# Kernel tuning notes

Hardware: AMD Instinct MI355X
Metric: run time of the kernel (lower is better)

The kernel has to match this reference:

```python
import jax, jax.numpy as jnp
import numpy as np

B, S, D = 2, 2048, 2048
H = 16
HD = D // (2 * H)          # 64, per-map head dim
LBDA_INIT = 0.8


def apply_rope_real(x, cos, sin):
    # x: [B, H, S, HD]; cos/sin: [S, HD//2]
    b, h, s, d = x.shape
    xr = x.reshape(b, h, s, d // 2, 2)
    x1, x2 = xr[..., 0], xr[..., 1]
    c = cos[None, None, :, :]
    sn = sin[None, None, :, :]
    o1 = x1 * c - x2 * sn
    o2 = x1 * sn + x2 * c
    return jnp.stack([o1, o2], axis=-1).reshape(b, h, s, d)


def setup_inputs() -> dict:
    key = jax.random.key(0)
    ks = jax.random.split(key, 6)
    x = jax.random.normal(ks[0], (B, S, D), dtype=jnp.float32)
    # causal additive mask [1,1,S,S]
    causal = jnp.tril(jnp.ones((S, S), dtype=bool))
    mask = jnp.where(causal, 0.0, -1e9).astype(jnp.float32)[None, None]
    # RoPE tables for half_head_dim = HD//2
    inv_freq = 1.0 / (10000.0 ** (jnp.arange(0, HD // 2, dtype=jnp.float32) / (HD // 2)))
    t = jnp.arange(S, dtype=jnp.float32)
    freqs = t[:, None] * inv_freq[None, :]          # [S, HD//2]
    cos, sin = jnp.cos(freqs), jnp.sin(freqs)
    W_qkv = jax.random.normal(ks[1], (D, HD * H * 2 * 3), dtype=jnp.float32) * (D ** -0.5)
    W_o = jax.random.normal(ks[2], (D, D), dtype=jnp.float32) * (D ** -0.5)
    ln_gamma = jnp.ones((H, 2 * HD), dtype=jnp.float32)
    ln_beta = jnp.zeros((H, 2 * HD), dtype=jnp.float32)
    lbda = jnp.float32(0.5)
    return {"x": x, "mask": mask, "cos": cos, "sin": sin, "W_qkv": W_qkv,
            "W_o": W_o, "ln_gamma": ln_gamma, "ln_beta": ln_beta, "lbda": lbda}


def reference(x, mask, cos, sin, W_qkv, W_o, ln_gamma, ln_beta, lbda):
    b, s, d = x.shape
    scale = HD ** -0.5
    qkv = x @ W_qkv                                  # [B, S, 6*H*HD]
    q, k, v = jnp.split(qkv, 3, axis=-1)
    # [B, S, H, 2*HD] -> [B, H, S, 2*HD]
    q = q.reshape(b, s, H, 2 * HD).transpose(0, 2, 1, 3)
    k = k.reshape(b, s, H, 2 * HD).transpose(0, 2, 1, 3)
    v = v.reshape(b, s, H, 2 * HD).transpose(0, 2, 1, 3)
    q1, q2 = jnp.split(q, 2, axis=-1)
    k1, k2 = jnp.split(k, 2, axis=-1)
    q1, k1 = apply_rope_real(q1, cos, sin), apply_rope_real(k1, cos, sin)
    q2, k2 = apply_rope_real(q2, cos, sin), apply_rope_real(k2, cos, sin)
    qk1 = jnp.einsum('bhqd,bhkd->bhqk', q1, k1) * scale + mask
    qk2 = jnp.einsum('bhqd,bhkd->bhqk', q2, k2) * scale + mask
    a = jax.nn.softmax(qk1, axis=-1) - lbda * jax.nn.softmax(qk2, axis=-1)
    out = jnp.einsum('bhqk,bhkd->bhqd', a, v)        # [B, H, S, 2*HD]
    # per-head LayerNorm over last dim
    mu = out.mean(-1, keepdims=True)
    var = out.var(-1, keepdims=True)
    out = (out - mu) * jax.lax.rsqrt(var + 1e-5)
    out = out * ln_gamma[None, :, None, :] + ln_beta[None, :, None, :]
    out = out * (1.0 - LBDA_INIT)
    out = out.transpose(0, 2, 1, 3).reshape(b, s, d)
    return out @ W_o
```

## Files before the change

kernel.cpp:

```cpp
#include <hip/hip_runtime.h>
#include <hip/hip_bf16.h>
#include <cstdint>
#include <cstddef>

#define S_LEN 2048
#define NHEAD 16
#define BATCH 2

typedef unsigned short u16;
typedef __attribute__((ext_vector_type(8))) unsigned short u16x8;
typedef __attribute__((ext_vector_type(8))) short s16x8;
typedef __attribute__((ext_vector_type(4))) float f32x4;

__device__ __forceinline__ u16 bfb(float x) {
    __hip_bfloat16 b = __float2bfloat16(x);
    u16 u; __builtin_memcpy(&u, &b, 2); return u;
}
__device__ __forceinline__ float bff(u16 u) {
    __hip_bfloat16 b; __builtin_memcpy(&b, &u, 2); return __bfloat162float(b);
}

#define BMFMA(A, B, C) __builtin_amdgcn_mfma_f32_16x16x32_bf16( \
    __builtin_bit_cast(s16x8, A), __builtin_bit_cast(s16x8, B), C, 0, 0, 0)

template<int MODE>
__global__ __launch_bounds__(256)
void gemm_bf16s(const float* __restrict__ A, const float* __restrict__ B,
                float* __restrict__ C, float* __restrict__ qo,
                u16* __restrict__ khh, u16* __restrict__ khl,
                u16* __restrict__ vhh, u16* __restrict__ vhl,
                const float* __restrict__ ct, const float* __restrict__ st,
                int M, int N, int K)
{
    __shared__ u16 Ah[128 * 40];
    __shared__ u16 Al[128 * 40];
    __shared__ u16 Bh[128 * 40];
    __shared__ u16 Bl[128 * 40];

    const int tid  = threadIdx.x;
    const int lane = tid & 63;
    const int wid  = tid >> 6;
    const int wrow = wid >> 1, wcol = wid & 1;
    const int m0 = blockIdx.y * 128, n0 = blockIdx.x * 128;
    const int l15 = lane & 15;
    const int lg  = lane >> 4;
    const int bkb = tid & 7;
    const int bng = tid >> 3;

    f32x4 acc[4][4];
    #pragma unroll
    for (int mt = 0; mt < 4; mt++)
        #pragma unroll
        for (int nt = 0; nt < 4; nt++)
            acc[mt][nt] = (f32x4){0.f, 0.f, 0.f, 0.f};

    for (int k0 = 0; k0 < K; k0 += 32) {
        float4 av[4], bv[4];
        int am[4], ak[4];
        #pragma unroll
        for (int f = 0; f < 4; f++) {
            const int ai = f * 256 + tid;
            am[f] = ai >> 3;
            ak[f] = (ai & 7) * 4;
            av[f] = *(const float4*)(A + (size_t)(m0 + am[f]) * K + k0 + ak[f]);
            bv[f] = *(const float4*)(B + (size_t)(k0 + bkb * 4 + f) * N + n0 + bng * 4);
        }
        __syncthreads();
        #pragma unroll
        for (int f = 0; f < 4; f++) {
            const float* ap = reinterpret_cast<const float*>(&av[f]);
            const int off = am[f] * 40 + ak[f];
            #pragma unroll
            for (int e = 0; e < 4; e++) {
                const u16 hu = bfb(ap[e]);
                Ah[off + e] = hu;
                Al[off + e] = bfb(ap[e] - bff(hu));
            }
        }
        #pragma unroll
        for (int e = 0; e < 4; e++) {
            const int off = (bng * 4 + e) * 40 + bkb * 4;
            #pragma unroll
            for (int f = 0; f < 4; f++) {
                const float x = reinterpret_cast<const float*>(&bv[f])[e];
                const u16 hu = bfb(x);
                Bh[off + f] = hu;
                Bl[off + f] = bfb(x - bff(hu));
            }
        }
        __syncthreads();

        u16x8 bh[4], bl[4];
        #pragma unroll
        for (int nt = 0; nt < 4; nt++) {
            const int off = (wcol * 64 + nt * 16 + l15) * 40 + lg * 8;
            bh[nt] = *(const u16x8*)&Bh[off];
            bl[nt] = *(const u16x8*)&Bl[off];
        }
        #pragma unroll
        for (int mt = 0; mt < 4; mt++) {
            const int off = (wrow * 64 + mt * 16 + l15) * 40 + lg * 8;
            const u16x8 ah = *(const u16x8*)&Ah[off];
            const u16x8 al = *(const u16x8*)&Al[off];
            #pragma unroll
            for (int nt = 0; nt < 4; nt++) {
                acc[mt][nt] = BMFMA(al, bh[nt], acc[mt][nt]);
                acc[mt][nt] = BMFMA(ah, bl[nt], acc[mt][nt]);
                acc[mt][nt] = BMFMA(ah, bh[nt], acc[mt][nt]);
            }
        }
    }

    #pragma unroll
    for (int mt = 0; mt < 4; mt++) {
        #pragma unroll
        for (int r = 0; r < 4; r++) {
            const int row = m0 + wrow * 64 + mt * 16 + lg * 4 + r;
            if (MODE == 0) {
                #pragma unroll
                for (int nt = 0; nt < 4; nt++) {
                    const int col = n0 + wcol * 64 + nt * 16 + l15;
                    C[(size_t)row * N + col] = acc[mt][nt][r];
                }
            } else {
                const int b = row >> 11, s = row & 2047;
                #pragma unroll
                for (int nt = 0; nt < 4; nt++) {
                    const int col = n0 + wcol * 64 + nt * 16 + l15;
                    const int which = col >> 11;
                    const int cc = col & 2047;
                    const int hh = cc >> 7, d = cc & 127;
                    float v = acc[mt][nt][r];
                    const float pv = __shfl_xor(v, 1);
                    if (which < 2) {
                        const int p = (d & 63) >> 1;
                        const float c  = ct[s * 32 + p];
                        const float sn = st[s * 32 + p];
                        v = (d & 1) ? (pv * sn + v * c) : (v * c - pv * sn);
                    }
                    const size_t idx =
                        ((size_t)(b * NHEAD + hh) * S_LEN + s) * 128 + d;
                    if (which == 0) {
                        qo[idx] = v;
                    } else if (which == 1) {
                        const u16 hu = bfb(v);
                        khh[idx] = hu;
                        khl[idx] = bfb(v - bff(hu));
                    } else {
                        const u16 hu = bfb(v);
                        vhh[idx] = hu;
                        vhl[idx] = bfb(v - bff(hu));
                    }
                }
            }
        }
    }
}

__global__ __launch_bounds__(256)
void transpose_v(const u16* __restrict__ vhh, const u16* __restrict__ vhl,
                 u16* __restrict__ vth, u16* __restrict__ vtl)
{
    __shared__ unsigned int T[64][130];
    const int tid = threadIdx.x;
    const int s0 = blockIdx.x * 64;
    const int bh = blockIdx.y;
    const size_t base = (size_t)bh * S_LEN * 128;

    #pragma unroll
    for (int i = 0; i < 4; i++) {
        const int f = i * 256 + tid;
        const int r = f >> 4, c8 = (f & 15) * 8;
        const u16x8 h = *(const u16x8*)(vhh + base + (size_t)(s0 + r) * 128 + c8);
        const u16x8 l = *(const u16x8*)(vhl + base + (size_t)(s0 + r) * 128 + c8);
        #pragma unroll
        for (int e = 0; e < 8; e++)
            T[r][c8 + e] = ((unsigned int)h[e] << 16) | l[e];
    }
    __syncthreads();

    const int d = tid >> 1, sc = (tid & 1) * 32;
    u16x8 oh[4], ol[4];
    #pragma unroll
    for (int j = 0; j < 32; j++) {
        const unsigned int w = T[sc + j][d];
        oh[j >> 3][j & 7] = (u16)(w >> 16);
        ol[j >> 3][j & 7] = (u16)(w & 0xffff);
    }
    const size_t ob = ((size_t)bh * 128 + d) * S_LEN + s0 + sc;
    #pragma unroll
    for (int k = 0; k < 4; k++) {
        *(u16x8*)(vth + ob + k * 8) = oh[k];
        *(u16x8*)(vtl + ob + k * 8) = ol[k];
    }
}

__global__ __launch_bounds__(256, 2)
void diff_attn_mfma(const float* __restrict__ qh,
                    const u16* __restrict__ khh, const u16* __restrict__ khl,
                    const u16* __restrict__ vth, const u16* __restrict__ vtl,
                    const float* __restrict__ gamma, const float* __restrict__ beta,
                    const float* __restrict__ lbda_p, float* __restrict__ att)
{
    __shared__ u16 sKh[64 * 128];
    __shared__ u16 sKl[64 * 128];
    __shared__ u16 sVh[128 * 64];
    __shared__ u16 sVl[128 * 64];
    __shared__ u16 sP[4][16 * 64];

    const int tid = threadIdx.x, lane = tid & 63, wid = tid >> 6;
    const int l15 = lane & 15, lg = lane >> 4;
    const int qt = blockIdx.x, h = blockIdx.y, b = blockIdx.z;
    const int bh = b * NHEAD + h;
    const int q0w = qt * 64 + wid * 16;

    u16x8 qfh[2][2], qfl[2][2];
    {
        const float* Qrow = qh + ((size_t)bh * S_LEN + q0w + l15) * 128;
        #pragma unroll
        for (int h12 = 0; h12 < 2; h12++)
            #pragma unroll
            for (int ks = 0; ks < 2; ks++) {
                const int d0 = h12 * 64 + ks * 32 + lg * 8;
                const float4 x = *(const float4*)(Qrow + d0);
                const float4 y = *(const float4*)(Qrow + d0 + 4);
                const float xs[8] = {x.x, x.y, x.z, x.w, y.x, y.y, y.z, y.w};
                u16x8 hh, ll;
                #pragma unroll
                for (int e = 0; e < 8; e++) {
                    const float v = xs[e] * 0.125f;
                    const u16 hu = bfb(v);
                    hh[e] = hu;
                    ll[e] = bfb(v - bff(hu));
                }
                qfh[h12][ks] = hh;
                qfl[h12][ks] = ll;
            }
    }

    f32x4 o1[8], o2[8];
    #pragma unroll
    for (int i = 0; i < 8; i++) {
        o1[i] = (f32x4){0.f, 0.f, 0.f, 0.f};
        o2[i] = (f32x4){0.f, 0.f, 0.f, 0.f};
    }
    float l1[4] = {0.f, 0.f, 0.f, 0.f}, l2[4] = {0.f, 0.f, 0.f, 0.f};

    for (int kt = 0; kt <= qt; kt++) {
        const int kv0 = kt * 64;
        u16x8 rkh[4], rkl[4], rvh[4], rvl[4];
        #pragma unroll
        for (int i = 0; i < 4; i++) {
            const int f = i * 256 + tid;
            {
                const int kv = f >> 4, blk = f & 15;
                const size_t g = ((size_t)bh * S_LEN + kv0 + kv) * 128 + blk * 8;
                rkh[i] = *(const u16x8*)(khh + g);
                rkl[i] = *(const u16x8*)(khl + g);
            }
            {
                const int dd = f >> 3, vb = f & 7;
                const size_t g = ((size_t)bh * 128 + dd) * S_LEN + kv0 + vb * 8;
                rvh[i] = *(const u16x8*)(vth + g);
                rvl[i] = *(const u16x8*)(vtl + g);
            }
        }
        __syncthreads();
        #pragma unroll
        for (int i = 0; i < 4; i++) {
            const int f = i * 256 + tid;
            {
                const int kv = f >> 4, blk = f & 15;
                const int a = kv * 128 + ((blk ^ (kv & 7)) * 8);
                *(u16x8*)&sKh[a] = rkh[i];
                *(u16x8*)&sKl[a] = rkl[i];
            }
            {
                const int dd = f >> 3, vb = f & 7;
                const int a = dd * 64 + ((vb ^ (dd & 7)) * 8);
                *(u16x8*)&sVh[a] = rvh[i];
                *(u16x8*)&sVl[a] = rvl[i];
            }
        }
        __syncthreads();

        f32x4 s1[4], s2[4];
        #pragma unroll
        for (int nt = 0; nt < 4; nt++) {
            s1[nt] = (f32x4){0.f, 0.f, 0.f, 0.f};
            s2[nt] = (f32x4){0.f, 0.f, 0.f, 0.f};
        }
        #pragma unroll
        for (int ks = 0; ks < 2; ks++)
            #pragma unroll
            for (int nt = 0; nt < 4; nt++) {
                const int kvr = nt * 16 + l15;
                const int cb = l15 & 7;
                {
                    const int a = kvr * 128 + (((ks * 4 + lg) ^ cb) * 8);
                    const u16x8 kbh = *(const u16x8*)&sKh[a];
                    const u16x8 kbl = *(const u16x8*)&sKl[a];
                    s1[nt] = BMFMA(qfl[0][ks], kbh, s1[nt]);
                    s1[nt] = BMFMA(qfh[0][ks], kbl, s1[nt]);
                    s1[nt] = BMFMA(qfh[0][ks], kbh, s1[nt]);
                }
                {
                    const int a = kvr * 128 + (((8 + ks * 4 + lg) ^ cb) * 8);
                    const u16x8 kbh = *(const u16x8*)&sKh[a];
                    const u16x8 kbl = *(const u16x8*)&sKl[a];
                    s2[nt] = BMFMA(qfl[1][ks], kbh, s2[nt]);
                    s2[nt] = BMFMA(qfh[1][ks], kbl, s2[nt]);
                    s2[nt] = BMFMA(qfh[1][ks], kbh, s2[nt]);
                }
            }

        const bool diag = (kt == qt);
        float p1[4][4], p2[4][4];
        #pragma unroll
        for (int nt = 0; nt < 4; nt++)
            #pragma unroll
            for (int r = 0; r < 4; r++) {
                float e1 = __expf(s1[nt][r]);
                float e2 = __expf(s2[nt][r]);
                if (diag) {
                    const int kv = kv0 + nt * 16 + l15;
                    const int qq = q0w + lg * 4 + r;
                    if (kv > qq) { e1 = 0.f; e2 = 0.f; }
                }
                p1[nt][r] = e1;
                p2[nt][r] = e2;
            }
        #pragma unroll
        for (int r = 0; r < 4; r++) {
            float a1 = p1[0][r] + p1[1][r] + p1[2][r] + p1[3][r];
            float a2 = p2[0][r] + p2[1][r] + p2[2][r] + p2[3][r];
            #pragma unroll
            for (int off = 1; off < 16; off <<= 1) {
                a1 += __shfl_xor(a1, off);
                a2 += __shfl_xor(a2, off);
            }
            l1[r] += a1;
            l2[r] += a2;
        }

        u16* myP = &sP[wid][0];
        #pragma unroll
        for (int nt = 0; nt < 4; nt++)
            #pragma unroll
            for (int r = 0; r < 4; r++) {
                const int q = lg * 4 + r, kv = l15 + nt * 16;
                myP[q * 64 + (((kv >> 3) ^ (q & 7)) * 8) + (kv & 7)] =
                    bfb(p1[nt][r]);
            }
        {
            u16x8 pf0 = *(const u16x8*)&myP[l15 * 64 + ((lg ^ (l15 & 7)) * 8)];
            u16x8 pf1 = *(const u16x8*)&myP[l15 * 64 + (((4 + lg) ^ (l15 & 7)) * 8)];
            #pragma unroll
            for (int nt = 0; nt < 8; nt++) {
                const int dr = nt * 16 + l15;
                const int cb = l15 & 7;
                {
                    const int a = dr * 64 + ((lg ^ cb) * 8);
                    o1[nt] = BMFMA(pf0, *(const u16x8*)&sVh[a], o1[nt]);
                    o1[nt] = BMFMA(pf0, *(const u16x8*)&sVl[a], o1[nt]);
                }
                {
                    const int a = dr * 64 + (((4 + lg) ^ cb) * 8);
                    o1[nt] = BMFMA(pf1, *(const u16x8*)&sVh[a], o1[nt]);
                    o1[nt] = BMFMA(pf1, *(const u16x8*)&sVl[a], o1[nt]);
                }
            }
        }
        #pragma unroll
        for (int nt = 0; nt < 4; nt++)
            #pragma unroll
            for (int r = 0; r < 4; r++) {
                const int q = lg * 4 + r, kv = l15 + nt * 16;
                myP[q * 64 + (((kv >> 3) ^ (q & 7)) * 8) + (kv & 7)] =
                    bfb(p2[nt][r]);
            }
        {
            u16x8 pf0 = *(const u16x8*)&myP[l15 * 64 + ((lg ^ (l15 & 7)) * 8)];
            u16x8 pf1 = *(const u16x8*)&myP[l15 * 64 + (((4 + lg) ^ (l15 & 7)) * 8)];
            #pragma unroll
            for (int nt = 0; nt < 8; nt++) {
                const int dr = nt * 16 + l15;
                const int cb = l15 & 7;
                {
                    const int a = dr * 64 + ((lg ^ cb) * 8);
                    o2[nt] = BMFMA(pf0, *(const u16x8*)&sVh[a], o2[nt]);
                    o2[nt] = BMFMA(pf0, *(const u16x8*)&sVl[a], o2[nt]);
                }
                {
                    const int a = dr * 64 + (((4 + lg) ^ cb) * 8);
                    o2[nt] = BMFMA(pf1, *(const u16x8*)&sVh[a], o2[nt]);
                    o2[nt] = BMFMA(pf1, *(const u16x8*)&sVl[a], o2[nt]);
                }
            }
        }
    }

    const float lam = lbda_p[0];
    float inv1[4], inv2[4];
    #pragma unroll
    for (int r = 0; r < 4; r++) {
        inv1[r] = 1.f / l1[r];
        inv2[r] = lam / l2[r];
    }
    float o[8][4];
    float sum[4] = {0.f, 0.f, 0.f, 0.f}, ssq[4] = {0.f, 0.f, 0.f, 0.f};
    #pragma unroll
    for (int nt = 0; nt < 8; nt++)
        #pragma unroll
        for (int r = 0; r < 4; r++) {
            const float v = o1[nt][r] * inv1[r] - o2[nt][r] * inv2[r];
            o[nt][r] = v;
            sum[r] += v;
            ssq[r] += v * v;
        }
    #pragma unroll
    for (int r = 0; r < 4; r++)
        #pragma unroll
        for (int off = 1; off < 16; off <<= 1) {
            sum[r] += __shfl_xor(sum[r], off);
            ssq[r] += __shfl_xor(ssq[r], off);
        }
    #pragma unroll
    for (int nt = 0; nt < 8; nt++) {
        const int d = nt * 16 + l15;
        const float gm = gamma[h * 128 + d];
        const float bt = beta[h * 128 + d];
        #pragma unroll
        for (int r = 0; r < 4; r++) {
            const float mu = sum[r] * (1.f / 128.f);
            const float var = ssq[r] * (1.f / 128.f) - mu * mu;
            const float rs = rsqrtf(var + 1e-5f);
            const int s = q0w + lg * 4 + r;
            att[((size_t)(b * S_LEN + s)) * 2048 + h * 128 + d] =
                ((o[nt][r] - mu) * rs * gm + bt) * 0.2f;
        }
    }
}

extern "C" void kernel_launch(void* const* d_in, const int* in_sizes, int n_in,
                              void* d_out, int out_size, void* d_ws, size_t ws_size,
                              hipStream_t stream)
{
    const float* x     = (const float*)d_in[0];
    const float* cosT  = (const float*)d_in[2];
    const float* sinT  = (const float*)d_in[3];
    const float* W_qkv = (const float*)d_in[4];
    const float* W_o   = (const float*)d_in[5];
    const float* gamma = (const float*)d_in[6];
    const float* beta  = (const float*)d_in[7];
    const float* lbda  = (const float*)d_in[8];
    float* out = (float*)d_out;

    float* ws = (float*)d_ws;
    const size_t HS = (size_t)BATCH * NHEAD * S_LEN * 128;
    float* qh  = ws;
    u16* khh   = (u16*)(ws + HS);
    u16* khl   = khh + HS;
    u16* vhh   = (u16*)(ws + 2 * HS);
    u16* vhl   = vhh + HS;
    u16* vth   = (u16*)(ws + 3 * HS);
    u16* vtl   = vth + HS;
    float* att = ws + 2 * HS;

    {
        dim3 grid(6144 / 128, 4096 / 128);
        gemm_bf16s<1><<<grid, 256, 0, stream>>>(x, W_qkv, nullptr, qh,
                                                khh, khl, vhh, vhl,
                                                cosT, sinT, 4096, 6144, 2048);
    }
    {
        dim3 grid(S_LEN / 64, BATCH * NHEAD);
        transpose_v<<<grid, 256, 0, stream>>>(vhh, vhl, vth, vtl);
    }
    {
        dim3 grid(S_LEN / 64, NHEAD, BATCH);
        diff_attn_mfma<<<grid, 256, 0, stream>>>(qh, khh, khl, vth, vtl,
                                                 gamma, beta, lbda, att);
    }
    {
        dim3 grid(2048 / 128, 4096 / 128);
        gemm_bf16s<0><<<grid, 256, 0, stream>>>(att, W_o, out, nullptr,
                                                nullptr, nullptr, nullptr, nullptr,
                                                nullptr, nullptr, 4096, 2048, 2048);
    }
}
```

Before: 981.7 us.

## Pre-split GEMM operands into bf16 hi/lo buffers instead of per-tile conversion

Adds conversion kernels that split x and a transposed W_o into bf16 high/low pairs once, and makes the attention kernel emit its output directly as bf16 hi/lo. The QKV and output GEMMs then load pre-split bf16 operands with vectorized LDS stores, removing repeated float-to-bf16 splitting inside every tile iteration. This costs extra passes over x and W_o and reuses workspace regions whose earlier contents are already dead.

```diff
diff --git a/kernel.cpp b/kernel.cpp
--- a/kernel.cpp
+++ b/kernel.cpp
@@ -9,6 +9,7 @@
 
 typedef unsigned short u16;
 typedef __attribute__((ext_vector_type(8))) unsigned short u16x8;
+typedef __attribute__((ext_vector_type(4))) unsigned short u16x4;
 typedef __attribute__((ext_vector_type(8))) short s16x8;
 typedef __attribute__((ext_vector_type(4))) float f32x4;
 
@@ -23,15 +24,64 @@
 #define BMFMA(A, B, C) __builtin_amdgcn_mfma_f32_16x16x32_bf16( \
     __builtin_bit_cast(s16x8, A), __builtin_bit_cast(s16x8, B), C, 0, 0, 0)
 
-template<int MODE>
 __global__ __launch_bounds__(256)
-void gemm_bf16s(const float* __restrict__ A, const float* __restrict__ B,
-                float* __restrict__ C, float* __restrict__ qo,
-                u16* __restrict__ khh, u16* __restrict__ khl,
-                u16* __restrict__ vhh, u16* __restrict__ vhl,
-                const float* __restrict__ ct, const float* __restrict__ st,
-                int M, int N, int K)
+void convert_split(const float* __restrict__ in, u16* __restrict__ oh,
+                   u16* __restrict__ ol)
 {
+    const size_t base = ((size_t)blockIdx.x * 256 + threadIdx.x) * 8;
+    const float4 a = *(const float4*)(in + base);
+    const float4 b = *(const float4*)(in + base + 4);
+    const float xs[8] = {a.x, a.y, a.z, a.w, b.x, b.y, b.z, b.w};
+    u16x8 hh, ll;
+    #pragma unroll
+    for (int e = 0; e < 8; e++) {
+        const u16 hu = bfb(xs[e]);
+        hh[e] = hu;
+        ll[e] = bfb(xs[e] - bff(hu));
+    }
+    *(u16x8*)(oh + base) = hh;
+    *(u16x8*)(ol + base) = ll;
+}
+
+__global__ __launch_bounds__(256)
+void convert_wot(const float* __restrict__ W, u16* __restrict__ bh,
+                 u16* __restrict__ bl)
+{
+    __shared__ float T[64][65];
+    const int tid = threadIdx.x;
+    const int n0 = blockIdx.x * 64, k0 = blockIdx.y * 64;
+    #pragma unroll
+    for (int i = 0; i < 4; i++) {
+        const int c = i * 256 + tid;
+        const int r = c >> 4, n4 = (c & 15) * 4;
+        *(float4*)&T[r][n4] = *(const float4*)(W + (size_t)(k0 + r) * 2048 + n0 + n4);
+    }
+    __syncthreads();
+    #pragma unroll
+    for (int i = 0; i < 4; i++) {
+        const int c = i * 256 + tid;
+        const int n = c >> 4, k4 = (c & 15) * 4;
+        u16 h[4], l[4];
+        #pragma unroll
+        for (int j = 0; j < 4; j++) {
+            const float v = T[k4 + j][n];
+            h[j] = bfb(v);
+            l[j] = bfb(v - bff(h[j]));
+        }
+        const size_t off = (size_t)(n0 + n) * 2048 + k0 + k4;
+        *(u16x4*)(bh + off) = (u16x4){h[0], h[1], h[2], h[3]};
+        *(u16x4*)(bl + off) = (u16x4){l[0], l[1], l[2], l[3]};
+    }
+}
+
+__global__ __launch_bounds__(256)
+void gemm_qkv(const u16* __restrict__ xh, const u16* __restrict__ xl,
+              const float* __restrict__ B, float* __restrict__ qo,
+              u16* __restrict__ khh, u16* __restrict__ khl,
+              u16* __restrict__ vhh, u16* __restrict__ vhl,
+              const float* __restrict__ ct, const float* __restrict__ st)
+{
+    const int K = 2048, N = 6144;
     __shared__ u16 Ah[128 * 40];
     __shared__ u16 Al[128 * 40];
     __shared__ u16 Bh[128 * 40];
@@ -55,38 +105,41 @@
             acc[mt][nt] = (f32x4){0.f, 0.f, 0.f, 0.f};
 
     for (int k0 = 0; k0 < K; k0 += 32) {
-        float4 av[4], bv[4];
-        int am[4], ak[4];
-        #pragma unroll
-        for (int f = 0; f < 4; f++) {
-            const int ai = f * 256 + tid;
-            am[f] = ai >> 3;
-            ak[f] = (ai & 7) * 4;
-            av[f] = *(const float4*)(A + (size_t)(m0 + am[f]) * K + k0 + ak[f]);
+        u16x8 rah[2], ral[2];
+        int arow[2], ak8[2];
+        #pragma unroll
+        for (int i = 0; i < 2; i++) {
+            const int c = i * 256 + tid;
+            arow[i] = c >> 2;
+            ak8[i] = (c & 3) * 8;
+            const size_t g = (size_t)(m0 + arow[i]) * K + k0 + ak8[i];
+            rah[i] = *(const u16x8*)(xh + g);
+            ral[i] = *(const u16x8*)(xl + g);
+        }
+        float4 bv[4];
+        #pragma unroll
+        for (int f = 0; f < 4; f++)
             bv[f] = *(const float4*)(B + (size_t)(k0 + bkb * 4 + f) * N + n0 + bng * 4);
-        }
+
         __syncthreads();
         #pragma unroll
-        for (int f = 0; f < 4; f++) {
-            const float* ap = reinterpret_cast<const float*>(&av[f]);
-            const int off = am[f] * 40 + ak[f];
-            #pragma unroll
-            for (int e = 0; e < 4; e++) {
-                const u16 hu = bfb(ap[e]);
-                Ah[off + e] = hu;
-                Al[off + e] = bfb(ap[e] - bff(hu));
-            }
+        for (int i = 0; i < 2; i++) {
+            const int off = arow[i] * 40 + ak8[i];
+            *(u16x8*)&Ah[off] = rah[i];
+            *(u16x8*)&Al[off] = ral[i];
         }
         #pragma unroll
         for (int e = 0; e < 4; e++) {
-            const int off = (bng * 4 + e) * 40 + bkb * 4;
+            u16 h[4], l[4];
             #pragma unroll
             for (int f = 0; f < 4; f++) {
                 const float x = reinterpret_cast<const float*>(&bv[f])[e];
-                const u16 hu = bfb(x);
-                Bh[off + f] = hu;
-                Bl[off + f] = bfb(x - bff(hu));
-            }
+                h[f] = bfb(x);
+                l[f] = bfb(x - bff(h[f]));
+            }
+            const int off = (bng * 4 + e) * 40 + bkb * 4;
+            *(u16x4*)&Bh[off] = (u16x4){h[0], h[1], h[2], h[3]};
+            *(u16x4*)&Bl[off] = (u16x4){l[0], l[1], l[2], l[3]};
         }
         __syncthreads();
 
@@ -116,45 +169,122 @@
         #pragma unroll
         for (int r = 0; r < 4; r++) {
             const int row = m0 + wrow * 64 + mt * 16 + lg * 4 + r;
-            if (MODE == 0) {
-                #pragma unroll
-                for (int nt = 0; nt < 4; nt++) {
-                    const int col = n0 + wcol * 64 + nt * 16 + l15;
-                    C[(size_t)row * N + col] = acc[mt][nt][r];
-                }
-            } else {
-                const int b = row >> 11, s = row & 2047;
-                #pragma unroll
-                for (int nt = 0; nt < 4; nt++) {
-                    const int col = n0 + wcol * 64 + nt * 16 + l15;
-                    const int which = col >> 11;
-                    const int cc = col & 2047;
-                    const int hh = cc >> 7, d = cc & 127;
-                    float v = acc[mt][nt][r];
-                    const float pv = __shfl_xor(v, 1);
-                    if (which < 2) {
-                        const int p = (d & 63) >> 1;
-                        const float c  = ct[s * 32 + p];
-                        const float sn = st[s * 32 + p];
-                        v = (d & 1) ? (pv * sn + v * c) : (v * c - pv * sn);
-                    }
-                    const size_t idx =
-                        ((size_t)(b * NHEAD + hh) * S_LEN + s) * 128 + d;
-                    if (which == 0) {
-                        qo[idx] = v;
-                    } else if (which == 1) {
-                        const u16 hu = bfb(v);
-                        khh[idx] = hu;
-                        khl[idx] = bfb(v - bff(hu));
-                    } else {
-                        const u16 hu = bfb(v);
-                        vhh[idx] = hu;
-                        vhl[idx] = bfb(v - bff(hu));
-                    }
-                }
-            }
-        }
-    }
+            const int b = row >> 11, s = row & 2047;
+            #pragma unroll
+            for (int nt = 0; nt < 4; nt++) {
+                const int col = n0 + wcol * 64 + nt * 16 + l15;
+                const int which = col >> 11;
+                const int cc = col & 2047;
+                const int hh = cc >> 7, d = cc & 127;
+                float v = acc[mt][nt][r];
+                const float pv = __shfl_xor(v, 1);
+                if (which < 2) {
+                    const int p = (d & 63) >> 1;
+                    const float c  = ct[s * 32 + p];
+                    const float sn = st[s * 32 + p];
+                    v = (d & 1) ? (pv * sn + v * c) : (v * c - pv * sn);
+                }
+                const size_t idx = ((size_t)(b * NHEAD + hh) * S_LEN + s) * 128 + d;
+                if (which == 0) {
+                    qo[idx] = v;
+                } else if (which == 1) {
+                    const u16 hu = bfb(v);
+                    khh[idx] = hu;
+                    khl[idx] = bfb(v - bff(hu));
+                } else {
+                    const u16 hu = bfb(v);
+                    vhh[idx] = hu;
+                    vhl[idx] = bfb(v - bff(hu));
+                }
+            }
+        }
+    }
+}
+
+__global__ __launch_bounds__(256)
+void gemm_out(const u16* __restrict__ ah_, const u16* __restrict__ al_,
+              const u16* __restrict__ bth, const u16* __restrict__ btl,
+              float* __restrict__ C)
+{
+    const int K = 2048, N = 2048;
+    __shared__ u16 Ah[128 * 40];
+    __shared__ u16 Al[128 * 40];
+    __shared__ u16 Bh[128 * 40];
+    __shared__ u16 Bl[128 * 40];
+
+    const int tid  = threadIdx.x;
+    const int lane = tid & 63;
+    const int wid  = tid >> 6;
+    const int wrow = wid >> 1, wcol = wid & 1;
+    const int m0 = blockIdx.y * 128, n0 = blockIdx.x * 128;
+    const int l15 = lane & 15;
+    const int lg  = lane >> 4;
+
+    f32x4 acc[4][4];
+    #pragma unroll
+    for (int mt = 0; mt < 4; mt++)
+        #pragma unroll
+        for (int nt = 0; nt < 4; nt++)
+            acc[mt][nt] = (f32x4){0.f, 0.f, 0.f, 0.f};
+
+    for (int k0 = 0; k0 < K; k0 += 32) {
+        u16x8 rah[2], ral[2], rbh[2], rbl[2];
+        int row[2], k8[2];
+        #pragma unroll
+        for (int i = 0; i < 2; i++) {
+            const int c = i * 256 + tid;
+            row[i] = c >> 2;
+            k8[i] = (c & 3) * 8;
+            const size_t ga = (size_t)(m0 + row[i]) * K + k0 + k8[i];
+            const size_t gb = (size_t)(n0 + row[i]) * K + k0 + k8[i];
+            rah[i] = *(const u16x8*)(ah_ + ga);
+            ral[i] = *(const u16x8*)(al_ + ga);
+            rbh[i] = *(const u16x8*)(bth + gb);
+            rbl[i] = *(const u16x8*)(btl + gb);
+        }
+        __syncthreads();
+        #pragma unroll
+        for (int i = 0; i < 2; i++) {
+            const int off = row[i] * 40 + k8[i];
+            *(u16x8*)&Ah[off] = rah[i];
+            *(u16x8*)&Al[off] = ral[i];
+            *(u16x8*)&Bh[off] = rbh[i];
+            *(u16x8*)&Bl[off] = rbl[i];
+        }
+        __syncthreads();
+
+        u16x8 bh[4], bl[4];
+        #pragma unroll
+        for (int nt = 0; nt < 4; nt++) {
+            const int off = (wcol * 64 + nt * 16 + l15) * 40 + lg * 8;
+            bh[nt] = *(const u16x8*)&Bh[off];
+            bl[nt] = *(const u16x8*)&Bl[off];
+        }
+        #pragma unroll
+        for (int mt = 0; mt < 4; mt++) {
+            const int off = (wrow * 64 + mt * 16 + l15) * 40 + lg * 8;
+            const u16x8 ah = *(const u16x8*)&Ah[off];
+            const u16x8 al = *(const u16x8*)&Al[off];
+            #pragma unroll
+            for (int nt = 0; nt < 4; nt++) {
+                acc[mt][nt] = BMFMA(al, bh[nt], acc[mt][nt]);
+                acc[mt][nt] = BMFMA(ah, bl[nt], acc[mt][nt]);
+                acc[mt][nt] = BMFMA(ah, bh[nt], acc[mt][nt]);
+            }
+        }
+    }
+
+    #pragma unroll
+    for (int mt = 0; mt < 4; mt++)
+        #pragma unroll
+        for (int r = 0; r < 4; r++) {
+            const int row = m0 + wrow * 64 + mt * 16 + lg * 4 + r;
+            #pragma unroll
+            for (int nt = 0; nt < 4; nt++) {
+                const int col = n0 + wcol * 64 + nt * 16 + l15;
+                C[(size_t)row * N + col] = acc[mt][nt][r];
+            }
+        }
 }
 
 __global__ __launch_bounds__(256)
@@ -200,7 +330,8 @@
                     const u16* __restrict__ khh, const u16* __restrict__ khl,
                     const u16* __restrict__ vth, const u16* __restrict__ vtl,
                     const float* __restrict__ gamma, const float* __restrict__ beta,
-                    const float* __restrict__ lbda_p, float* __restrict__ att)
+                    const float* __restrict__ lbda_p,
+                    u16* __restrict__ atth, u16* __restrict__ attl)
 {
     __shared__ u16 sKh[64 * 128];
     __shared__ u16 sKl[64 * 128];
@@ -436,8 +567,11 @@
             const float var = ssq[r] * (1.f / 128.f) - mu * mu;
             const float rs = rsqrtf(var + 1e-5f);
             const int s = q0w + lg * 4 + r;
-            att[((size_t)(b * S_LEN + s)) * 2048 + h * 128 + d] =
-                ((o[nt][r] - mu) * rs * gm + bt) * 0.2f;
+            const float v = ((o[nt][r] - mu) * rs * gm + bt) * 0.2f;
+            const size_t idx = ((size_t)(b * S_LEN + s)) * 2048 + h * 128 + d;
+            const u16 hu = bfb(v);
+            atth[idx] = hu;
+            attl[idx] = bfb(v - bff(hu));
         }
     }
 }
@@ -463,15 +597,20 @@
     u16* khl   = khh + HS;
     u16* vhh   = (u16*)(ws + 2 * HS);
     u16* vhl   = vhh + HS;
+    u16* xh    = (u16*)(ws + 3 * HS);
+    u16* xl    = xh + HS;
     u16* vth   = (u16*)(ws + 3 * HS);
     u16* vtl   = vth + HS;
-    float* att = ws + 2 * HS;
-
+    u16* atth  = (u16*)(ws + 2 * HS);
+    u16* attl  = atth + HS;
+    u16* woth  = (u16*)(ws + HS);
+    u16* wotl  = woth + (size_t)2048 * 2048;
+
+    convert_split<<<4096, 256, 0, stream>>>(x, xh, xl);
     {
         dim3 grid(6144 / 128, 4096 / 128);
-        gemm_bf16s<1><<<grid, 256, 0, stream>>>(x, W_qkv, nullptr, qh,
-                                                khh, khl, vhh, vhl,
-                                                cosT, sinT, 4096, 6144, 2048);
+        gemm_qkv<<<grid, 256, 0, stream>>>(xh, xl, W_qkv, qh,
+                                           khh, khl, vhh, vhl, cosT, sinT);
     }
     {
         dim3 grid(S_LEN / 64, BATCH * NHEAD);
@@ -480,12 +619,14 @@
     {
         dim3 grid(S_LEN / 64, NHEAD, BATCH);
         diff_attn_mfma<<<grid, 256, 0, stream>>>(qh, khh, khl, vth, vtl,
-                                                 gamma, beta, lbda, att);
+                                                 gamma, beta, lbda, atth, attl);
+    }
+    {
+        dim3 grid(2048 / 64, 2048 / 64);
+        convert_wot<<<grid, 256, 0, stream>>>(W_o, woth, wotl);
     }
     {
         dim3 grid(2048 / 128, 4096 / 128);
-        gemm_bf16s<0><<<grid, 256, 0, stream>>>(att, W_o, out, nullptr,
-                                                nullptr, nullptr, nullptr, nullptr,
-                                                nullptr, nullptr, 4096, 2048, 2048);
-    }
-}
+        gemm_out<<<grid, 256, 0, stream>>>(atth, attl, woth, wotl, out);
+    }
+}
```

Result: no change. 994.5 us (+1.3%).
